# Kernel optimization log

Measured on AMD Instinct MI355X. Metric: run time of the kernel, lower is better.

## Reference

```python
import jax, jax.numpy as jnp
import numpy as np

N_NODES = 100000
N_EDGES = 1250000
D_IN = 64
D_OUT = 64


def setup_inputs() -> dict:
    key = jax.random.key(0)
    k1, k2, k3 = jax.random.split(key, 3)
    x = jax.random.normal(k1, (N_NODES, D_IN), dtype=jnp.float32)
    edge_index = jax.random.randint(k2, (2, N_EDGES), 0, N_NODES, dtype=jnp.int64)
    # MLP([2*in, out]) -> single Linear(2*in, out) followed by ReLU
    W = jax.random.normal(k3, (2 * D_IN, D_OUT), dtype=jnp.float32) / np.sqrt(2 * D_IN)
    b = jnp.zeros((D_OUT,), dtype=jnp.float32)
    return {"x": x, "edge_index": edge_index, "W": W, "b": b}


def reference(x, edge_index, W, b):
    # EdgeConv: message(x_i, x_j) = relu(Linear(cat([x_i, x_j - x_i]))),
    # mean-aggregated at target node i.
    src = edge_index[0]  # j (source)
    dst = edge_index[1]  # i (target, aggregation index)
    x_i = x[dst]                                  # [E, D_IN]
    x_j = x[src]                                  # [E, D_IN]
    feat = jnp.concatenate([x_i, x_j - x_i], axis=-1)  # [E, 2*D_IN]
    h = jax.nn.relu(feat @ W + b)                 # [E, D_OUT]
    n = x.shape[0]
    summed = jax.ops.segment_sum(h, dst, num_segments=n)            # [N, D_OUT]
    count = jax.ops.segment_sum(jnp.ones((h.shape[0],), h.dtype), dst, num_segments=n)
    return summed / jnp.maximum(count, 1.0)[:, None]
```

## Files before the change

### kernel.cpp

```cpp
#include <hip/hip_runtime.h>
#include <hip/hip_bf16.h>

#define N_NODES 100000
#define N_EDGES 1250000
#define BNODES 128
#define NB ((N_NODES + BNODES - 1) / BNODES)
#define CAP 2560
#define PBLK 768
#define EPB ((N_EDGES + PBLK - 1) / PBLK)

typedef float f32x4 __attribute__((ext_vector_type(4)));
typedef short bf16x8 __attribute__((ext_vector_type(8)));

static __device__ __forceinline__ float bf2f(unsigned short u) {
    union { unsigned int i; float f; } v; v.i = ((unsigned int)u) << 16; return v.f;
}
static __device__ __forceinline__ unsigned short f2bf(float f) {
    union { float f; unsigned int i; } v; v.f = f;
    unsigned int x = v.i;
    return (unsigned short)((x + 0x7FFFu + ((x >> 16) & 1u)) >> 16);
}

__global__ __launch_bounds__(256) void prep_frags(const float* __restrict__ W,
                                                  unsigned short* __restrict__ Bfrag,
                                                  int* __restrict__ cursor) {
    int t = blockIdx.x * 256 + threadIdx.x;
    if (t < NB) cursor[t] = 0;
    if (t >= 8192) return;
    int f = t >> 9;
    int l = (t >> 3) & 63;
    int j = t & 7;
    int c = f >> 1, s = f & 1;
    int d = ((l >> 4) << 3) + j + 32 * s;
    int kcol = c * 16 + (l & 15);
    float v = (kcol < 64) ? (W[d * 64 + kcol] - W[(d + 64) * 64 + kcol])
                          : W[(d + 64) * 64 + (kcol - 64)];
    Bfrag[(size_t)f * 512 + l * 8 + j] = f2bf(v);
}

__global__ __launch_bounds__(256) void node_mfma(
    const float* __restrict__ x, const unsigned short* __restrict__ Bfrag,
    const float* __restrict__ b,
    unsigned short* __restrict__ y1, unsigned short* __restrict__ y2)
{
    int wid = (blockIdx.x * 256 + threadIdx.x) >> 6;
    int base = wid * 16;
    if (base >= N_NODES) return;
    int l = threadIdx.x & 63;
    int lo16 = l & 15, grp = l >> 4;

    bf16x8 bf[16];
    const uint4* bp = (const uint4*)Bfrag;
    #pragma unroll
    for (int f = 0; f < 16; ++f) {
        union { uint4 u; bf16x8 s; } cv;
        cv.u = bp[f * 64 + l];
        bf[f] = cv.s;
    }

    const float* xp = x + (size_t)(base + lo16) * 64 + (grp << 3);
    bf16x8 afr[2];
    #pragma unroll
    for (int s = 0; s < 2; ++s) {
        float4 v0 = *(const float4*)(xp + 32 * s);
        float4 v1 = *(const float4*)(xp + 32 * s + 4);
        bf16x8 a;
        a[0] = (short)f2bf(v0.x); a[1] = (short)f2bf(v0.y);
        a[2] = (short)f2bf(v0.z); a[3] = (short)f2bf(v0.w);
        a[4] = (short)f2bf(v1.x); a[5] = (short)f2bf(v1.y);
        a[6] = (short)f2bf(v1.z); a[7] = (short)f2bf(v1.w);
        afr[s] = a;
    }

    f32x4 acc[8];
    #pragma unroll
    for (int c = 0; c < 8; ++c) {
        float bias = (c < 4) ? b[c * 16 + lo16] : 0.0f;
        acc[c] = (f32x4){bias, bias, bias, bias};
    }

    #pragma unroll
    for (int c = 0; c < 8; ++c) {
        acc[c] = __builtin_amdgcn_mfma_f32_16x16x32_bf16(afr[0], bf[c * 2 + 0], acc[c], 0, 0, 0);
        acc[c] = __builtin_amdgcn_mfma_f32_16x16x32_bf16(afr[1], bf[c * 2 + 1], acc[c], 0, 0, 0);
    }

    #pragma unroll
    for (int c = 0; c < 8; ++c) {
        unsigned short* yp = (c < 4) ? y1 : y2;
        int colbase = (c & 3) * 16 + lo16;
        #pragma unroll
        for (int r = 0; r < 4; ++r) {
            int node = base + grp * 4 + r;
            yp[(size_t)node * 64 + colbase] = f2bf(acc[c][r]);
        }
    }
}

__global__ __launch_bounds__(256) void partition2(
    const int* __restrict__ ei,
    int* __restrict__ cursor, int* __restrict__ bins)
{
    __shared__ int h[NB];
    __shared__ int base[NB];

    int tid = threadIdx.x;
    int bid = blockIdx.x;
    int e0 = bid * EPB;
    int e1 = e0 + EPB; if (e1 > N_EDGES) e1 = N_EDGES;

    int sm = 0;
    #pragma unroll
    for (int t = 1; t <= 15; t += 2) sm |= ei[t];
    bool is64 = (sm == 0);

    for (int t = tid; t < NB; t += 256) h[t] = 0;
    __syncthreads();

    for (int e = e0 + tid; e < e1; e += 256) {
        int i = is64 ? ei[2 * (N_EDGES + e)] : ei[N_EDGES + e];
        atomicAdd(&h[i >> 7], 1);
    }
    __syncthreads();

    int shift = (bid * 263) % NB;
    for (int t = tid; t < NB; t += 256) {
        int bkt = t + shift; if (bkt >= NB) bkt -= NB;
        int c = h[bkt];
        base[bkt] = c ? atomicAdd(&cursor[bkt], c) : 0;
    }
    __syncthreads();
    for (int t = tid; t < NB; t += 256) h[t] = 0;
    __syncthreads();

    for (int e = e0 + tid; e < e1; e += 256) {
        int j, i;
        if (is64) { j = ei[2 * e];  i = ei[2 * (N_EDGES + e)]; }
        else      { j = ei[e];      i = ei[N_EDGES + e]; }
        int bkt = i >> 7;
        int pos = base[bkt] + atomicAdd(&h[bkt], 1);
        if (pos < CAP)
            bins[(size_t)bkt * CAP + pos] = ((i & 127) << 17) | j;
    }
}

__global__ __launch_bounds__(512) void bucket_all(
    const int* __restrict__ cursor, const int* __restrict__ bins,
    const unsigned short* __restrict__ y1, const unsigned short* __restrict__ y2,
    float* __restrict__ out)
{
    __shared__ int entries[CAP];
    __shared__ int sorted[CAP];
    __shared__ int h[BNODES], st[BNODES], cur[BNODES];

    int bkt = blockIdx.x;
    int n0 = bkt * BNODES;
    int nvalid = N_NODES - n0; if (nvalid > BNODES) nvalid = BNODES;
    int tid = threadIdx.x;

    if (tid < BNODES) h[tid] = 0;
    __syncthreads();

    int ecnt = cursor[bkt]; if (ecnt > CAP) ecnt = CAP;
    const int* ebase = bins + (size_t)bkt * CAP;
    for (int t = tid; t < ecnt; t += 512) {
        int e = ebase[t];
        entries[t] = e;
        atomicAdd(&h[e >> 17], 1);
    }
    __syncthreads();

    if (tid < BNODES) st[tid] = h[tid];
    __syncthreads();
    for (int off = 1; off < BNODES; off <<= 1) {
        int v = 0;
        if (tid < BNODES && tid >= off) v = st[tid - off];
        __syncthreads();
        if (tid < BNODES) st[tid] += v;
        __syncthreads();
    }
    if (tid < BNODES) { int e = st[tid] - h[tid]; st[tid] = e; cur[tid] = e; }
    __syncthreads();

    for (int t = tid; t < ecnt; t += 512) {
        int e = entries[t];
        int pos = atomicAdd(&cur[e >> 17], 1);
        sorted[pos] = e & 0x1FFFF;
    }
    __syncthreads();

    int g = tid >> 4;
    int q = tid & 15;
    for (int r = 0; r < 4; ++r) {
        int nl = g * 4 + r;
        if (nl >= nvalid) continue;
        int gn = n0 + nl;
        int rs = st[nl], d = h[nl];
        ushort4 a = *(const ushort4*)(y1 + (size_t)gn * 64 + q * 4);
        float a0 = bf2f(a.x), a1 = bf2f(a.y), a2 = bf2f(a.z), a3 = bf2f(a.w);
        float s0 = 0.f, s1 = 0.f, s2 = 0.f, s3 = 0.f;
        int k = 0;
        for (; k + 4 <= d; k += 4) {
            int j0 = sorted[rs + k], j1 = sorted[rs + k + 1];
            int j2 = sorted[rs + k + 2], j3 = sorted[rs + k + 3];
            ushort4 c0 = *(const ushort4*)(y2 + (size_t)j0 * 64 + q * 4);
            ushort4 c1 = *(const ushort4*)(y2 + (size_t)j1 * 64 + q * 4);
            ushort4 c2 = *(const ushort4*)(y2 + (size_t)j2 * 64 + q * 4);
            ushort4 c3 = *(const ushort4*)(y2 + (size_t)j3 * 64 + q * 4);
            s0 += fmaxf(a0 + bf2f(c0.x), 0.f); s1 += fmaxf(a1 + bf2f(c0.y), 0.f);
            s2 += fmaxf(a2 + bf2f(c0.z), 0.f); s3 += fmaxf(a3 + bf2f(c0.w), 0.f);
            s0 += fmaxf(a0 + bf2f(c1.x), 0.f); s1 += fmaxf(a1 + bf2f(c1.y), 0.f);
            s2 += fmaxf(a2 + bf2f(c1.z), 0.f); s3 += fmaxf(a3 + bf2f(c1.w), 0.f);
            s0 += fmaxf(a0 + bf2f(c2.x), 0.f); s1 += fmaxf(a1 + bf2f(c2.y), 0.f);
            s2 += fmaxf(a2 + bf2f(c2.z), 0.f); s3 += fmaxf(a3 + bf2f(c2.w), 0.f);
            s0 += fmaxf(a0 + bf2f(c3.x), 0.f); s1 += fmaxf(a1 + bf2f(c3.y), 0.f);
            s2 += fmaxf(a2 + bf2f(c3.z), 0.f); s3 += fmaxf(a3 + bf2f(c3.w), 0.f);
        }
        for (; k < d; ++k) {
            int j0 = sorted[rs + k];
            ushort4 c0 = *(const ushort4*)(y2 + (size_t)j0 * 64 + q * 4);
            s0 += fmaxf(a0 + bf2f(c0.x), 0.f); s1 += fmaxf(a1 + bf2f(c0.y), 0.f);
            s2 += fmaxf(a2 + bf2f(c0.z), 0.f); s3 += fmaxf(a3 + bf2f(c0.w), 0.f);
        }
        float inv = 1.0f / fmaxf((float)d, 1.0f);
        *((float4*)(out + (size_t)gn * 64) + q) =
            make_float4(s0 * inv, s1 * inv, s2 * inv, s3 * inv);
    }
}

extern "C" void kernel_launch(void* const* d_in, const int* in_sizes, int n_in,
                              void* d_out, int out_size, void* d_ws, size_t ws_size,
                              hipStream_t stream) {
    const float* x = (const float*)d_in[0];
    const int*   ei = (const int*)d_in[1];
    const float* W = (const float*)d_in[2];
    const float* b = (const float*)d_in[3];
    float* out = (float*)d_out;

    char* ws = (char*)d_ws;
    unsigned short* Bfrag  = (unsigned short*)(ws);
    int*          cursor   = (int*)(ws + 36864);
    unsigned short* y1     = (unsigned short*)(ws + 65536);
    unsigned short* y2     = (unsigned short*)(ws + 65536 + 12800000);
    int*          bins     = (int*)(ws + 65536 + 2 * (size_t)12800000);

    prep_frags<<<32, 256, 0, stream>>>(W, Bfrag, cursor);
    node_mfma<<<(N_NODES / 16 + 3) / 4, 256, 0, stream>>>(x, Bfrag, b, y1, y2);
    partition2<<<PBLK, 256, 0, stream>>>(ei, cursor, bins);
    bucket_all<<<NB, 512, 0, stream>>>(cursor, bins, y1, y2, out);
}
```

Measured before the change: 162.8 us.

## Fuse node MFMA with edge histogram and replace atomic cursors with column scan

The node-level MFMA projection and the per-block destination histogram now run in one launch as separate block ranges, so the edge counting overlaps with the dense compute. Global atomic cursor reservation is replaced by a per-block histogram matrix that a new scan kernel prefix-sums column-wise. This gives deterministic offsets and removes the global atomics. Edge index reads are also vectorised to two edges per thread. The cost is an extra kernel launch, an extra pass that writes and re-reads the histogram matrix, and a second full read of the destination indices.

```diff
diff --git a/kernel.cpp b/kernel.cpp
--- a/kernel.cpp
+++ b/kernel.cpp
@@ -6,8 +6,10 @@
 #define BNODES 128
 #define NB ((N_NODES + BNODES - 1) / BNODES)
 #define CAP 2560
-#define PBLK 768
-#define EPB ((N_EDGES + PBLK - 1) / PBLK)
+#define HB 768
+#define EPB ((N_EDGES + HB - 1) / HB)
+#define NBP 800
+#define MFMA_BLOCKS 1563
 
 typedef float f32x4 __attribute__((ext_vector_type(4)));
 typedef short bf16x8 __attribute__((ext_vector_type(8)));
@@ -20,12 +22,16 @@
     unsigned int x = v.i;
     return (unsigned short)((x + 0x7FFFu + ((x >> 16) & 1u)) >> 16);
 }
+static __device__ __forceinline__ bool detect_is64(const int* __restrict__ ei) {
+    int sm = 0;
+    #pragma unroll
+    for (int t = 1; t <= 15; t += 2) sm |= ei[t];
+    return sm == 0;
+}
 
 __global__ __launch_bounds__(256) void prep_frags(const float* __restrict__ W,
-                                                  unsigned short* __restrict__ Bfrag,
-                                                  int* __restrict__ cursor) {
+                                                  unsigned short* __restrict__ Bfrag) {
     int t = blockIdx.x * 256 + threadIdx.x;
-    if (t < NB) cursor[t] = 0;
     if (t >= 8192) return;
     int f = t >> 9;
     int l = (t >> 3) & 63;
@@ -38,114 +44,143 @@
     Bfrag[(size_t)f * 512 + l * 8 + j] = f2bf(v);
 }
 
-__global__ __launch_bounds__(256) void node_mfma(
+__global__ __launch_bounds__(256) void mfma_and_hist(
     const float* __restrict__ x, const unsigned short* __restrict__ Bfrag,
     const float* __restrict__ b,
-    unsigned short* __restrict__ y1, unsigned short* __restrict__ y2)
+    unsigned short* __restrict__ y1, unsigned short* __restrict__ y2,
+    const int* __restrict__ ei, int* __restrict__ H)
 {
-    int wid = (blockIdx.x * 256 + threadIdx.x) >> 6;
-    int base = wid * 16;
-    if (base >= N_NODES) return;
-    int l = threadIdx.x & 63;
-    int lo16 = l & 15, grp = l >> 4;
-
-    bf16x8 bf[16];
-    const uint4* bp = (const uint4*)Bfrag;
+    if (blockIdx.x < MFMA_BLOCKS) {
+        int wid = (blockIdx.x << 2) + (threadIdx.x >> 6);
+        int base = wid * 16;
+        if (base >= N_NODES) return;
+        int l = threadIdx.x & 63;
+        int lo16 = l & 15, grp = l >> 4;
+
+        bf16x8 bf[16];
+        const uint4* bp = (const uint4*)Bfrag;
+        #pragma unroll
+        for (int f = 0; f < 16; ++f) {
+            union { uint4 u; bf16x8 s; } cv;
+            cv.u = bp[f * 64 + l];
+            bf[f] = cv.s;
+        }
+
+        const float* xp = x + (size_t)(base + lo16) * 64 + (grp << 3);
+        bf16x8 afr[2];
+        #pragma unroll
+        for (int s = 0; s < 2; ++s) {
+            float4 v0 = *(const float4*)(xp + 32 * s);
+            float4 v1 = *(const float4*)(xp + 32 * s + 4);
+            bf16x8 a;
+            a[0] = (short)f2bf(v0.x); a[1] = (short)f2bf(v0.y);
+            a[2] = (short)f2bf(v0.z); a[3] = (short)f2bf(v0.w);
+            a[4] = (short)f2bf(v1.x); a[5] = (short)f2bf(v1.y);
+            a[6] = (short)f2bf(v1.z); a[7] = (short)f2bf(v1.w);
+            afr[s] = a;
+        }
+
+        f32x4 acc[8];
+        #pragma unroll
+        for (int c = 0; c < 8; ++c) {
+            float bias = (c < 4) ? b[c * 16 + lo16] : 0.0f;
+            acc[c] = (f32x4){bias, bias, bias, bias};
+        }
+        #pragma unroll
+        for (int c = 0; c < 8; ++c) {
+            acc[c] = __builtin_amdgcn_mfma_f32_16x16x32_bf16(afr[0], bf[c * 2 + 0], acc[c], 0, 0, 0);
+            acc[c] = __builtin_amdgcn_mfma_f32_16x16x32_bf16(afr[1], bf[c * 2 + 1], acc[c], 0, 0, 0);
+        }
+        #pragma unroll
+        for (int c = 0; c < 8; ++c) {
+            unsigned short* yp = (c < 4) ? y1 : y2;
+            int colbase = (c & 3) * 16 + lo16;
+            #pragma unroll
+            for (int r = 0; r < 4; ++r) {
+                int node = base + grp * 4 + r;
+                yp[(size_t)node * 64 + colbase] = f2bf(acc[c][r]);
+            }
+        }
+        return;
+    }
+
+    __shared__ int h[NB];
+    int hb = blockIdx.x - MFMA_BLOCKS;
+    int tid = threadIdx.x;
+    int e0 = hb * EPB;
+    int e1 = e0 + EPB; if (e1 > N_EDGES) e1 = N_EDGES;
+    bool is64 = detect_is64(ei);
+
+    for (int t = tid; t < NB; t += 256) h[t] = 0;
+    __syncthreads();
+
+    for (int e = e0 + 2 * tid; e < e1; e += 512) {
+        int d0, d1;
+        if (is64) { int4 d = *(const int4*)&ei[2 * (N_EDGES + e)]; d0 = d.x; d1 = d.z; }
+        else      { int2 d = *(const int2*)&ei[N_EDGES + e];       d0 = d.x; d1 = d.y; }
+        atomicAdd(&h[d0 >> 7], 1);
+        atomicAdd(&h[d1 >> 7], 1);
+    }
+    __syncthreads();
+    for (int t = tid; t < NB; t += 256) H[hb * NBP + t] = h[t];
+}
+
+__global__ __launch_bounds__(512) void scan_cols(int* __restrict__ H,
+                                                 int* __restrict__ cnt) {
+    int w = blockIdx.x * 8 + (threadIdx.x >> 6);
+    if (w >= NB) return;
+    int lane = threadIdx.x & 63;
+    int running = 0;
     #pragma unroll
-    for (int f = 0; f < 16; ++f) {
-        union { uint4 u; bf16x8 s; } cv;
-        cv.u = bp[f * 64 + l];
-        bf[f] = cv.s;
-    }
-
-    const float* xp = x + (size_t)(base + lo16) * 64 + (grp << 3);
-    bf16x8 afr[2];
-    #pragma unroll
-    for (int s = 0; s < 2; ++s) {
-        float4 v0 = *(const float4*)(xp + 32 * s);
-        float4 v1 = *(const float4*)(xp + 32 * s + 4);
-        bf16x8 a;
-        a[0] = (short)f2bf(v0.x); a[1] = (short)f2bf(v0.y);
-        a[2] = (short)f2bf(v0.z); a[3] = (short)f2bf(v0.w);
-        a[4] = (short)f2bf(v1.x); a[5] = (short)f2bf(v1.y);
-        a[6] = (short)f2bf(v1.z); a[7] = (short)f2bf(v1.w);
-        afr[s] = a;
-    }
-
-    f32x4 acc[8];
-    #pragma unroll
-    for (int c = 0; c < 8; ++c) {
-        float bias = (c < 4) ? b[c * 16 + lo16] : 0.0f;
-        acc[c] = (f32x4){bias, bias, bias, bias};
-    }
-
-    #pragma unroll
-    for (int c = 0; c < 8; ++c) {
-        acc[c] = __builtin_amdgcn_mfma_f32_16x16x32_bf16(afr[0], bf[c * 2 + 0], acc[c], 0, 0, 0);
-        acc[c] = __builtin_amdgcn_mfma_f32_16x16x32_bf16(afr[1], bf[c * 2 + 1], acc[c], 0, 0, 0);
-    }
-
-    #pragma unroll
-    for (int c = 0; c < 8; ++c) {
-        unsigned short* yp = (c < 4) ? y1 : y2;
-        int colbase = (c & 3) * 16 + lo16;
-        #pragma unroll
-        for (int r = 0; r < 4; ++r) {
-            int node = base + grp * 4 + r;
-            yp[(size_t)node * 64 + colbase] = f2bf(acc[c][r]);
-        }
-    }
-}
-
-__global__ __launch_bounds__(256) void partition2(
-    const int* __restrict__ ei,
-    int* __restrict__ cursor, int* __restrict__ bins)
+    for (int it = 0; it < HB / 64; ++it) {
+        int bb = it * 64 + lane;
+        int v = H[bb * NBP + w];
+        int s = v;
+        #pragma unroll
+        for (int off = 1; off < 64; off <<= 1) {
+            int t = __shfl_up(s, off, 64);
+            if (lane >= off) s += t;
+        }
+        H[bb * NBP + w] = running + s - v;
+        running += __shfl(s, 63, 64);
+    }
+    if (lane == 0) cnt[w] = running;
+}
+
+__global__ __launch_bounds__(256) void scatter_part(
+    const int* __restrict__ ei, const int* __restrict__ H,
+    int* __restrict__ bins)
 {
-    __shared__ int h[NB];
     __shared__ int base[NB];
-
-    int tid = threadIdx.x;
-    int bid = blockIdx.x;
-    int e0 = bid * EPB;
+    __shared__ int cur[NB];
+    int hb = blockIdx.x, tid = threadIdx.x;
+    int e0 = hb * EPB;
     int e1 = e0 + EPB; if (e1 > N_EDGES) e1 = N_EDGES;
-
-    int sm = 0;
-    #pragma unroll
-    for (int t = 1; t <= 15; t += 2) sm |= ei[t];
-    bool is64 = (sm == 0);
-
-    for (int t = tid; t < NB; t += 256) h[t] = 0;
-    __syncthreads();
-
-    for (int e = e0 + tid; e < e1; e += 256) {
-        int i = is64 ? ei[2 * (N_EDGES + e)] : ei[N_EDGES + e];
-        atomicAdd(&h[i >> 7], 1);
-    }
-    __syncthreads();
-
-    int shift = (bid * 263) % NB;
-    for (int t = tid; t < NB; t += 256) {
-        int bkt = t + shift; if (bkt >= NB) bkt -= NB;
-        int c = h[bkt];
-        base[bkt] = c ? atomicAdd(&cursor[bkt], c) : 0;
-    }
-    __syncthreads();
-    for (int t = tid; t < NB; t += 256) h[t] = 0;
-    __syncthreads();
-
-    for (int e = e0 + tid; e < e1; e += 256) {
-        int j, i;
-        if (is64) { j = ei[2 * e];  i = ei[2 * (N_EDGES + e)]; }
-        else      { j = ei[e];      i = ei[N_EDGES + e]; }
-        int bkt = i >> 7;
-        int pos = base[bkt] + atomicAdd(&h[bkt], 1);
-        if (pos < CAP)
-            bins[(size_t)bkt * CAP + pos] = ((i & 127) << 17) | j;
+    bool is64 = detect_is64(ei);
+
+    for (int t = tid; t < NB; t += 256) { base[t] = H[hb * NBP + t]; cur[t] = 0; }
+    __syncthreads();
+
+    for (int e = e0 + 2 * tid; e < e1; e += 512) {
+        int d0, d1, s0, s1;
+        if (is64) {
+            int4 d = *(const int4*)&ei[2 * (N_EDGES + e)];
+            int4 s = *(const int4*)&ei[2 * e];
+            d0 = d.x; d1 = d.z; s0 = s.x; s1 = s.z;
+        } else {
+            int2 d = *(const int2*)&ei[N_EDGES + e];
+            int2 s = *(const int2*)&ei[e];
+            d0 = d.x; d1 = d.y; s0 = s.x; s1 = s.y;
+        }
+        int b0 = d0 >> 7, p0 = base[b0] + atomicAdd(&cur[b0], 1);
+        if (p0 < CAP) bins[(size_t)b0 * CAP + p0] = ((d0 & 127) << 17) | s0;
+        int b1 = d1 >> 7, p1 = base[b1] + atomicAdd(&cur[b1], 1);
+        if (p1 < CAP) bins[(size_t)b1 * CAP + p1] = ((d1 & 127) << 17) | s1;
     }
 }
 
 __global__ __launch_bounds__(512) void bucket_all(
-    const int* __restrict__ cursor, const int* __restrict__ bins,
+    const int* __restrict__ cnt, const int* __restrict__ bins,
     const unsigned short* __restrict__ y1, const unsigned short* __restrict__ y2,
     float* __restrict__ out)
 {
@@ -161,7 +196,7 @@
     if (tid < BNODES) h[tid] = 0;
     __syncthreads();
 
-    int ecnt = cursor[bkt]; if (ecnt > CAP) ecnt = CAP;
+    int ecnt = cnt[bkt]; if (ecnt > CAP) ecnt = CAP;
     const int* ebase = bins + (size_t)bkt * CAP;
     for (int t = tid; t < ecnt; t += 512) {
         int e = ebase[t];
@@ -238,14 +273,16 @@
     float* out = (float*)d_out;
 
     char* ws = (char*)d_ws;
-    unsigned short* Bfrag  = (unsigned short*)(ws);
-    int*          cursor   = (int*)(ws + 36864);
-    unsigned short* y1     = (unsigned short*)(ws + 65536);
-    unsigned short* y2     = (unsigned short*)(ws + 65536 + 12800000);
-    int*          bins     = (int*)(ws + 65536 + 2 * (size_t)12800000);
-
-    prep_frags<<<32, 256, 0, stream>>>(W, Bfrag, cursor);
-    node_mfma<<<(N_NODES / 16 + 3) / 4, 256, 0, stream>>>(x, Bfrag, b, y1, y2);
-    partition2<<<PBLK, 256, 0, stream>>>(ei, cursor, bins);
-    bucket_all<<<NB, 512, 0, stream>>>(cursor, bins, y1, y2, out);
-}
+    unsigned short* Bfrag = (unsigned short*)(ws);
+    int*            cnt   = (int*)(ws + 36864);
+    int*            H     = (int*)(ws + 65536);
+    unsigned short* y1    = (unsigned short*)(ws + (4u << 20));
+    unsigned short* y2    = (unsigned short*)(ws + (4u << 20) + 12800000);
+    int*            bins  = (int*)(ws + (32u << 20));
+
+    prep_frags<<<32, 256, 0, stream>>>(W, Bfrag);
+    mfma_and_hist<<<MFMA_BLOCKS + HB, 256, 0, stream>>>(x, Bfrag, b, y1, y2, ei, H);
+    scan_cols<<<(NB + 7) / 8, 512, 0, stream>>>(H, cnt);
+    scatter_part<<<HB, 256, 0, stream>>>(ei, H, bins);
+    bucket_all<<<NB, 512, 0, stream>>>(cnt, bins, y1, y2, out);
+}
```

Result: faster. 157.5 us (-3.3%).
